# Performance work log

Hardware: AMD Instinct MI355X
Metric: run time of the kernel (lower is better)

Reference implementation:

```python
import jax, jax.numpy as jnp
import numpy as np
from jax import lax

NUM_NODES = 100000
FEAT = 256
RANK = 16
NNZ = 4000000
NUM_HE = 125000  # num_hyperedges == num_edges_total
K = 2000000      # int(0.5 * NNZ)


def setup_inputs() -> dict:
    key = jax.random.key(0)
    ks = jax.random.split(key, 6)
    x = jax.random.normal(ks[0], (NUM_NODES, FEAT), dtype=jnp.float32)
    W = jax.random.normal(ks[1], (RANK, FEAT), dtype=jnp.float32)
    edge_factors = jax.random.normal(ks[2], (NUM_HE, RANK), dtype=jnp.float32)
    V_idx = jax.random.randint(ks[3], (NNZ,), 0, NUM_NODES, dtype=jnp.int32)
    E_idx = jax.random.randint(ks[4], (NNZ,), 0, NUM_HE, dtype=jnp.int32)
    edge_ids = jax.random.randint(ks[5], (NUM_HE,), 0, NUM_HE, dtype=jnp.int32)
    return {"x": x, "W": W, "edge_factors": edge_factors,
            "V_idx": V_idx, "E_idx": E_idx, "edge_ids": edge_ids, "k": K}


def _segment_mean(vals, seg_ids, num_segments):
    s = jax.ops.segment_sum(vals, seg_ids, num_segments=num_segments)
    c = jax.ops.segment_sum(jnp.ones_like(vals), seg_ids, num_segments=num_segments)
    return s / jnp.maximum(c, 1.0)


def reference(x, W, edge_factors, V_idx, E_idx, edge_ids, k):
    # node_proj(x): [N, rank]; gather per-incidence node and edge factors, dot product
    proj = x @ W.T                                  # [N, rank]
    ef = edge_factors[edge_ids[E_idx]]              # [nnz, rank]
    logits = jnp.sum(proj[V_idx] * ef, axis=-1)     # [nnz]
    scores = jax.nn.sigmoid(logits)

    # is_test=True path: deterministic top-k keep set
    _, keep_ids = lax.top_k(scores, k)
    hard = jnp.zeros_like(scores).at[keep_ids].set(1.0)
    # straight-through: forward == hard, gradient flows through scores where hard==1
    soft = hard + (scores - lax.stop_gradient(scores)) * hard

    edge_probs = _segment_mean(lax.stop_gradient(scores), E_idx, NUM_HE)
    edge_soft = _segment_mean(soft, E_idx, NUM_HE)
    edge_hard = (_segment_mean(hard, E_idx, NUM_HE) > 0).astype(jnp.float32)
    return scores, soft, hard, edge_probs, edge_soft, edge_hard
```

## Files before the change

### kernel.cpp

```cpp
#include <hip/hip_runtime.h>
#include <math.h>

#define FEAT 256
#define RANKK 16
#define PRJ_NODES 16
#define CAND_CAP 131072
#define TIE_CAP 2048
#define NBK_MAX 512

typedef unsigned long long u64;

static __device__ __forceinline__ u64 pack_pair(unsigned e_low, unsigned bits, unsigned idx) {
    return ((u64)e_low << 56) | ((u64)bits << 26) | (u64)idx;
}

__global__ __launch_bounds__(256) void proj_kernel(const float* __restrict__ x,
        const float* __restrict__ Wm, float* __restrict__ proj, int n_nodes) {
    __shared__ float Ws[RANKK][FEAT + 4];
    __shared__ float Xs[PRJ_NODES][FEAT + 4];
    const float4* x4 = (const float4*)x;
    const float4* w4 = (const float4*)Wm;
    for (int t = threadIdx.x; t < RANKK * (FEAT / 4); t += 256) {
        int r = t >> 6, j4 = t & 63;
        *(float4*)&Ws[r][j4 * 4] = w4[t];
    }
    int nodeBase = blockIdx.x * PRJ_NODES;
    for (int t = threadIdx.x; t < PRJ_NODES * (FEAT / 4); t += 256) {
        int n = t >> 6, j4 = t & 63;
        int node = nodeBase + n;
        float4 v = make_float4(0.f, 0.f, 0.f, 0.f);
        if (node < n_nodes) v = x4[(size_t)node * (FEAT / 4) + j4];
        *(float4*)&Xs[n][j4 * 4] = v;
    }
    __syncthreads();
    int n = threadIdx.x >> 4, r = threadIdx.x & 15;
    int node = nodeBase + n;
    if (node >= n_nodes) return;
    double acc = 0.0;
    #pragma unroll 8
    for (int j4 = 0; j4 < FEAT / 4; ++j4) {
        float4 xv = *(const float4*)&Xs[n][j4 * 4];
        float4 wv = *(const float4*)&Ws[r][j4 * 4];
        acc += (double)xv.x * (double)wv.x + (double)xv.y * (double)wv.y
             + (double)xv.z * (double)wv.z + (double)xv.w * (double)wv.w;
    }
    proj[(size_t)node * RANKK + r] = (float)acc;
}

__global__ void gather_ef(const float4* __restrict__ ef, const int* __restrict__ edge_ids,
                          float4* __restrict__ ef2, int nhe) {
    int t = blockIdx.x * blockDim.x + threadIdx.x;
    if (t >= nhe * 4) return;
    int e = t >> 2, c = t & 3;
    ef2[(size_t)e * 4 + c] = ef[(size_t)edge_ids[e] * 4 + c];
}

__global__ void ehist_kernel(const int* __restrict__ E_idx, unsigned* __restrict__ bucketCnt,
                             int nnz, int nb) {
    __shared__ unsigned h[NBK_MAX];
    for (int t = threadIdx.x; t < NBK_MAX; t += blockDim.x) h[t] = 0;
    __syncthreads();
    for (int i = blockIdx.x * blockDim.x + threadIdx.x; i < nnz; i += gridDim.x * blockDim.x)
        atomicAdd(&h[((unsigned)E_idx[i]) >> 8], 1u);
    __syncthreads();
    for (int t = threadIdx.x; t < nb; t += blockDim.x)
        if (h[t]) atomicAdd(&bucketCnt[t], h[t]);
}

__global__ void bucket_scan(const unsigned* __restrict__ bucketCnt,
                            unsigned* __restrict__ bucketBase, unsigned* __restrict__ cursor,
                            int nb, int nnz) {
    __shared__ unsigned s[NBK_MAX];
    int t = threadIdx.x;
    unsigned c = (t < nb) ? bucketCnt[t] : 0u;
    s[t] = c;
    __syncthreads();
    for (int off = 1; off < NBK_MAX; off <<= 1) {
        unsigned v = (t >= off) ? s[t - off] : 0u;
        __syncthreads();
        s[t] += v;
        __syncthreads();
    }
    unsigned excl = s[t] - c;
    if (t < nb) { bucketBase[t] = excl; cursor[t] = excl; }
    if (t == 0) bucketBase[nb] = (unsigned)nnz;
}

__global__ __launch_bounds__(256) void score_kernel(
        const float4* __restrict__ proj4, const float4* __restrict__ ef4,
        const int2* __restrict__ V2, const int2* __restrict__ E2,
        float2* __restrict__ scores2, unsigned* __restrict__ hist1g,
        int npair, int nnz) {
    __shared__ unsigned h[4096];
    for (int t = threadIdx.x; t < 4096; t += 256) h[t] = 0;
    __syncthreads();
    unsigned r1016 = 0, r1015 = 0, r0 = 0;
    int stride = gridDim.x * 256;
    for (int i = blockIdx.x * 256 + threadIdx.x; i < npair; i += stride) {
        int2 v = V2[i];
        int2 e = E2[i];
        float4 a0 = proj4[(size_t)v.x * 4 + 0];
        float4 a1 = proj4[(size_t)v.x * 4 + 1];
        float4 a2 = proj4[(size_t)v.x * 4 + 2];
        float4 a3 = proj4[(size_t)v.x * 4 + 3];
        float4 b0 = proj4[(size_t)v.y * 4 + 0];
        float4 b1 = proj4[(size_t)v.y * 4 + 1];
        float4 b2 = proj4[(size_t)v.y * 4 + 2];
        float4 b3 = proj4[(size_t)v.y * 4 + 3];
        float4 f0 = ef4[(size_t)e.x * 4 + 0];
        float4 f1 = ef4[(size_t)e.x * 4 + 1];
        float4 f2 = ef4[(size_t)e.x * 4 + 2];
        float4 f3 = ef4[(size_t)e.x * 4 + 3];
        float4 g0 = ef4[(size_t)e.y * 4 + 0];
        float4 g1 = ef4[(size_t)e.y * 4 + 1];
        float4 g2 = ef4[(size_t)e.y * 4 + 2];
        float4 g3 = ef4[(size_t)e.y * 4 + 3];
        double acc0 = (double)a0.x * f0.x + (double)a0.y * f0.y + (double)a0.z * f0.z + (double)a0.w * f0.w
                    + (double)a1.x * f1.x + (double)a1.y * f1.y + (double)a1.z * f1.z + (double)a1.w * f1.w
                    + (double)a2.x * f2.x + (double)a2.y * f2.y + (double)a2.z * f2.z + (double)a2.w * f2.w
                    + (double)a3.x * f3.x + (double)a3.y * f3.y + (double)a3.z * f3.z + (double)a3.w * f3.w;
        double acc1 = (double)b0.x * g0.x + (double)b0.y * g0.y + (double)b0.z * g0.z + (double)b0.w * g0.w
                    + (double)b1.x * g1.x + (double)b1.y * g1.y + (double)b1.z * g1.z + (double)b1.w * g1.w
                    + (double)b2.x * g2.x + (double)b2.y * g2.y + (double)b2.z * g2.z + (double)b2.w * g2.w
                    + (double)b3.x * g3.x + (double)b3.y * g3.y + (double)b3.z * g3.z + (double)b3.w * g3.w;
        float s0 = (float)(1.0 / (1.0 + exp(-acc0)));
        float s1 = (float)(1.0 / (1.0 + exp(-acc1)));
        scores2[i] = make_float2(s0, s1);
        unsigned bb0 = __float_as_uint(s0) >> 20;
        unsigned bb1 = __float_as_uint(s1) >> 20;
        if (bb0 == 1016) ++r1016; else if (bb0 == 1015) ++r1015;
        else if (bb0 == 0) ++r0; else atomicAdd(&h[bb0], 1u);
        if (bb1 == 1016) ++r1016; else if (bb1 == 1015) ++r1015;
        else if (bb1 == 0) ++r0; else atomicAdd(&h[bb1], 1u);
    }
    if ((nnz & 1) && blockIdx.x == 0 && threadIdx.x == 0) {
        int i = nnz - 1;
        const int* Vi = (const int*)V2;
        const int* Ei = (const int*)E2;
        const float* pr = (const float*)proj4;
        const float* fr = (const float*)ef4;
        int v = Vi[i], e = Ei[i];
        double acc = 0.0;
        for (int r = 0; r < RANKK; ++r)
            acc += (double)pr[(size_t)v * RANKK + r] * (double)fr[(size_t)e * RANKK + r];
        float s = (float)(1.0 / (1.0 + exp(-acc)));
        ((float*)scores2)[i] = s;
        atomicAdd(&hist1g[__float_as_uint(s) >> 20], 1u);
    }
    if (r1016) atomicAdd(&h[1016], r1016);
    if (r1015) atomicAdd(&h[1015], r1015);
    if (r0) atomicAdd(&h[0], r0);
    __syncthreads();
    for (int t = threadIdx.x; t < 4096; t += 256)
        if (h[t]) atomicAdd(&hist1g[t], h[t]);
}

#define PB_CHUNK 8192
__global__ __launch_bounds__(256) void pair_build(const int* __restrict__ E_idx,
        const float* __restrict__ scores, u64* __restrict__ pairs,
        unsigned* __restrict__ cursor, int nnz, int nb) {
    __shared__ unsigned bh[NBK_MAX];
    for (int t = threadIdx.x; t < NBK_MAX; t += 256) bh[t] = 0;
    __syncthreads();
    int base = blockIdx.x * PB_CHUNK;
    int nE = nnz - base;
    if (nE > PB_CHUNK) nE = PB_CHUNK;
    for (int o = threadIdx.x; o < nE; o += 256)
        atomicAdd(&bh[((unsigned)E_idx[base + o]) >> 8], 1u);
    __syncthreads();
    for (int b = threadIdx.x; b < nb; b += 256) {
        unsigned c = bh[b];
        bh[b] = c ? atomicAdd(&cursor[b], c) : 0u;
    }
    __syncthreads();
    for (int o = threadIdx.x; o < nE; o += 256) {
        int i = base + o;
        unsigned e = (unsigned)E_idx[i];
        unsigned bits = __float_as_uint(scores[i]);
        unsigned pos = atomicAdd(&bh[e >> 8], 1u);
        pairs[pos] = pack_pair(e & 255u, bits, (unsigned)i);
    }
}

__global__ void scan1_kernel(const unsigned* __restrict__ hist,
                             unsigned* __restrict__ sel, const int* __restrict__ kptr) {
    __shared__ unsigned sfx[256];
    int t = threadIdx.x;
    unsigned local[16];
    unsigned s = 0;
    #pragma unroll
    for (int j = 0; j < 16; ++j) { local[j] = hist[t * 16 + j]; s += local[j]; }
    sfx[t] = s;
    __syncthreads();
    for (int off = 1; off < 256; off <<= 1) {
        unsigned add = (t + off < 256) ? sfx[t + off] : 0;
        __syncthreads();
        sfx[t] += add;
        __syncthreads();
    }
    unsigned krem = (unsigned)(*kptr);
    unsigned above = (t + 1 < 256) ? sfx[t + 1] : 0;
    if (above < krem && sfx[t] >= krem) {
        unsigned cum = above;
        int b = t * 16;
        for (int j = 15; j >= 0; --j) {
            unsigned cc = local[j];
            if (cum + cc >= krem) { b = t * 16 + j; break; }
            cum += cc;
        }
        sel[0] = krem - cum;
        sel[1] = ((unsigned)b) << 20;
    }
}

__global__ void compact_kernel(const float4* __restrict__ scores4,
                               const unsigned* __restrict__ sel,
                               uint2* __restrict__ cand, unsigned* __restrict__ candCount,
                               int n4, int nnz) {
    unsigned pref = sel[1] >> 20;
    int tid = blockIdx.x * blockDim.x + threadIdx.x;
    int stride = gridDim.x * blockDim.x;
    int lane = threadIdx.x & 63;
    int niter = (n4 + stride - 1) / stride;
    for (int kk = 0; kk < niter; ++kk) {
        int i = tid + kk * stride;
        bool inb = (i < n4);
        float4 sv = make_float4(0.f, 0.f, 0.f, 0.f);
        if (inb) sv = scores4[i];
        unsigned bb[4] = {__float_as_uint(sv.x), __float_as_uint(sv.y),
                          __float_as_uint(sv.z), __float_as_uint(sv.w)};
        #pragma unroll
        for (int q = 0; q < 4; ++q) {
            bool pred = inb && ((bb[q] >> 20) == pref);
            unsigned long long mask = __ballot(pred);
            if (mask) {
                int leader = __ffsll(mask) - 1;
                unsigned base = 0;
                if (lane == leader) base = atomicAdd(candCount, (unsigned)__popcll(mask));
                base = __shfl(base, leader, 64);
                if (pred) {
                    unsigned rank = __popcll(mask & ((1ull << lane) - 1ull));
                    unsigned pos = base + rank;
                    if (pos < CAND_CAP) cand[pos] = make_uint2(bb[q], (unsigned)(i * 4 + q));
                }
            }
        }
    }
    for (int i = n4 * 4 + tid; i < nnz; i += stride) {
        unsigned b = __float_as_uint(((const float*)scores4)[i]);
        if ((b >> 20) == pref) {
            unsigned pos = atomicAdd(candCount, 1u);
            if (pos < CAND_CAP) cand[pos] = make_uint2(b, (unsigned)i);
        }
    }
}

__global__ __launch_bounds__(256) void select_small(const uint2* __restrict__ cand,
                            const unsigned* __restrict__ candCount,
                            unsigned* __restrict__ sel, unsigned* __restrict__ tieList) {
    __shared__ unsigned h2[4096];
    __shared__ unsigned sfx[256];
    __shared__ unsigned sB2, sKrem2, sT, sM;
    __shared__ unsigned h3[256];
    __shared__ unsigned ties[TIE_CAP];
    __shared__ unsigned tcnt;
    int t = threadIdx.x;
    unsigned nc = *candCount;
    int n = (nc < CAND_CAP) ? (int)nc : CAND_CAP;
    unsigned krem = sel[0];
    unsigned pref = sel[1];

    for (int j = t; j < 4096; j += 256) h2[j] = 0;
    if (t == 0) tcnt = 0;
    __syncthreads();
    for (int j = t; j < n; j += 256) atomicAdd(&h2[(cand[j].x >> 8) & 0xFFF], 1u);
    __syncthreads();

    unsigned local[16];
    unsigned s = 0;
    #pragma unroll
    for (int j = 0; j < 16; ++j) { local[j] = h2[t * 16 + j]; s += local[j]; }
    sfx[t] = s;
    __syncthreads();
    for (int off = 1; off < 256; off <<= 1) {
        unsigned add = (t + off < 256) ? sfx[t + off] : 0;
        __syncthreads();
        sfx[t] += add;
        __syncthreads();
    }
    {
        unsigned above = (t + 1 < 256) ? sfx[t + 1] : 0;
        if (above < krem && sfx[t] >= krem) {
            unsigned cum = above;
            int b = t * 16;
            for (int j = 15; j >= 0; --j) {
                unsigned cc = local[j];
                if (cum + cc >= krem) { b = t * 16 + j; break; }
                cum += cc;
            }
            sB2 = (unsigned)b;
            sKrem2 = krem - cum;
        }
    }
    __syncthreads();

    h3[t] = 0;
    __syncthreads();
    unsigned b2 = sB2;
    for (int j = t; j < n; j += 256) {
        unsigned x = cand[j].x;
        if (((x >> 8) & 0xFFF) == b2) atomicAdd(&h3[x & 0xFF], 1u);
    }
    __syncthreads();
    sfx[t] = h3[t];
    __syncthreads();
    for (int off = 1; off < 256; off <<= 1) {
        unsigned add = (t + off < 256) ? sfx[t + off] : 0;
        __syncthreads();
        sfx[t] += add;
        __syncthreads();
    }
    {
        unsigned krem2 = sKrem2;
        unsigned above = (t + 1 < 256) ? sfx[t + 1] : 0;
        if (above < krem2 && sfx[t] >= krem2) {
            sT = pref | (b2 << 8) | (unsigned)t;
            sM = krem2 - above;
        }
    }
    __syncthreads();

    unsigned T = sT;
    for (int j = t; j < n; j += 256) {
        if (cand[j].x == T) {
            unsigned p = atomicAdd(&tcnt, 1u);
            if (p < TIE_CAP) ties[p] = cand[j].y;
        }
    }
    __syncthreads();
    if (t == 0) {
        unsigned cnt = (tcnt < TIE_CAP) ? tcnt : TIE_CAP;
        for (unsigned a = 1; a < cnt; ++a) {
            unsigned key = ties[a];
            int bpos = (int)a - 1;
            while (bpos >= 0 && ties[bpos] > key) { ties[bpos + 1] = ties[bpos]; --bpos; }
            ties[bpos + 1] = key;
        }
        unsigned m = sM;
        if (m > cnt) m = cnt;
        sel[2] = T;
        sel[3] = m;
        for (unsigned j = 0; j < m; ++j) tieList[j] = ties[j];
    }
}

__global__ __launch_bounds__(256) void edge_final(const u64* __restrict__ pairs,
        const unsigned* __restrict__ bucketBase, const unsigned* __restrict__ sel,
        const unsigned* __restrict__ tieList,
        float* __restrict__ eprob, float* __restrict__ esoft, float* __restrict__ ehard,
        int nhe) {
    __shared__ float ss[256];
    __shared__ unsigned cc[256];
    __shared__ unsigned hh[256];
    __shared__ unsigned ties[TIE_CAP];
    unsigned T = sel[2];
    unsigned m = sel[3];
    if (m > TIE_CAP) m = TIE_CAP;
    int t = threadIdx.x;
    ss[t] = 0.f; cc[t] = 0u; hh[t] = 0u;
    for (int j = t; j < (int)m; j += 256) ties[j] = tieList[j];
    __syncthreads();
    int b = blockIdx.x;
    unsigned n0 = bucketBase[b], n1 = bucketBase[b + 1];
    for (unsigned j = n0 + t; j < n1; j += 256) {
        u64 p = pairs[j];
        unsigned el = (unsigned)(p >> 56);
        unsigned bits = (unsigned)(p >> 26) & 0x3FFFFFFFu;
        atomicAdd(&ss[el], __uint_as_float(bits));
        atomicAdd(&cc[el], 1u);
        bool keep = bits > T;
        if (bits == T) {
            unsigned idx = (unsigned)(p & 0x3FFFFFFu);
            int lo = 0, hi = (int)m - 1;
            keep = false;
            while (lo <= hi) {
                int mid = (lo + hi) >> 1;
                unsigned v = ties[mid];
                if (v == idx) { keep = true; break; }
                if (v < idx) lo = mid + 1; else hi = mid - 1;
            }
        }
        if (keep) atomicAdd(&hh[el], 1u);
    }
    __syncthreads();
    int e = b * 256 + t;
    if (e < nhe) {
        float c = fmaxf((float)cc[t], 1.0f);
        eprob[e] = ss[t] / c;
        esoft[e] = (float)hh[t] / c;
        ehard[e] = (hh[t] > 0) ? 1.0f : 0.0f;
    }
}

__global__ __launch_bounds__(256) void write_hard(const float4* __restrict__ scores4,
                           const unsigned* __restrict__ sel,
                           const unsigned* __restrict__ tieList,
                           float4* __restrict__ hard4, float4* __restrict__ soft4,
                           int n4, int nnz) {
    __shared__ unsigned ties[TIE_CAP];
    unsigned T = sel[2];
    unsigned m = sel[3];
    if (m > TIE_CAP) m = TIE_CAP;
    for (int j = threadIdx.x; j < (int)m; j += blockDim.x) ties[j] = tieList[j];
    __syncthreads();
    int tid = blockIdx.x * blockDim.x + threadIdx.x;
    int stride = gridDim.x * blockDim.x;
    for (int i = tid; i < n4; i += stride) {
        float4 sv = scores4[i];
        unsigned bb[4] = {__float_as_uint(sv.x), __float_as_uint(sv.y),
                          __float_as_uint(sv.z), __float_as_uint(sv.w)};
        float hv[4];
        #pragma unroll
        for (int q = 0; q < 4; ++q) {
            bool keep = (bb[q] > T);
            if (bb[q] == T) {
                unsigned idx = (unsigned)(i * 4 + q);
                int lo = 0, hi = (int)m - 1;
                keep = false;
                while (lo <= hi) {
                    int mid = (lo + hi) >> 1;
                    unsigned v = ties[mid];
                    if (v == idx) { keep = true; break; }
                    if (v < idx) lo = mid + 1; else hi = mid - 1;
                }
            }
            hv[q] = keep ? 1.0f : 0.0f;
        }
        float4 outv = make_float4(hv[0], hv[1], hv[2], hv[3]);
        hard4[i] = outv;
        soft4[i] = outv;
    }
    const float* sc = (const float*)scores4;
    float* hard = (float*)hard4;
    float* soft = (float*)soft4;
    for (int i = n4 * 4 + tid; i < nnz; i += stride) {
        unsigned b = __float_as_uint(sc[i]);
        bool keep = (b > T);
        if (b == T) {
            unsigned idx = (unsigned)i;
            int lo = 0, hi = (int)m - 1;
            keep = false;
            while (lo <= hi) {
                int mid = (lo + hi) >> 1;
                unsigned v = ties[mid];
                if (v == idx) { keep = true; break; }
                if (v < idx) lo = mid + 1; else hi = mid - 1;
            }
        }
        float hvv = keep ? 1.0f : 0.0f;
        hard[i] = hvv;
        soft[i] = hvv;
    }
}

extern "C" void kernel_launch(void* const* d_in, const int* in_sizes, int n_in,
                              void* d_out, int out_size, void* d_ws, size_t ws_size,
                              hipStream_t stream) {
    const float* x        = (const float*)d_in[0];
    const float* Wm       = (const float*)d_in[1];
    const float* ef       = (const float*)d_in[2];
    const int*   V_idx    = (const int*)d_in[3];
    const int*   E_idx    = (const int*)d_in[4];
    const int*   edge_ids = (const int*)d_in[5];
    const int*   kptr     = (const int*)d_in[6];

    const int nnz     = in_sizes[3];
    const int nhe     = in_sizes[5];
    const int n_nodes = in_sizes[0] / FEAT;
    const int nb      = (nhe + 255) >> 8;

    float* out    = (float*)d_out;
    float* scores = out;
    float* soft   = out + (size_t)nnz;
    float* hard   = out + 2 * (size_t)nnz;
    float* eprob  = out + 3 * (size_t)nnz;
    float* esoft  = eprob + nhe;
    float* ehard  = esoft + nhe;

    u64*   pairs = (u64*)soft;
    uint2* cand  = (uint2*)eprob;

    char* w = (char*)d_ws;
    unsigned* hist1      = (unsigned*)w;
    unsigned* bucketCnt  = hist1 + 4096;
    unsigned* candCount  = bucketCnt + NBK_MAX;
    unsigned* sel        = candCount + 1;
    unsigned* tieList    = sel + 8;
    unsigned* bucketBase = tieList + TIE_CAP;
    unsigned* cursor     = bucketBase + NBK_MAX + 1;
    char* auxEnd = (char*)(cursor + NBK_MAX);
    size_t auxAligned = (((size_t)(auxEnd - w)) + 255) & ~(size_t)255;

    size_t ef2Bytes  = (size_t)nhe * RANKK * sizeof(float);
    size_t projBytes = (size_t)n_nodes * RANKK * sizeof(float);

    float* ef2;
    float* proj;
    if (ws_size >= auxAligned + ef2Bytes + projBytes) {
        ef2  = (float*)(w + auxAligned);
        proj = (float*)(w + auxAligned + ef2Bytes);
    } else {
        ef2  = hard;
        proj = hard + (size_t)nhe * RANKK;
    }

    hipMemsetAsync(w, 0, (size_t)(4096 + NBK_MAX + 1) * sizeof(unsigned), stream);

    ehist_kernel<<<128, 256, 0, stream>>>(E_idx, bucketCnt, nnz, nb);
    bucket_scan<<<1, NBK_MAX, 0, stream>>>(bucketCnt, bucketBase, cursor, nb, nnz);
    gather_ef<<<(nhe * 4 + 255) / 256, 256, 0, stream>>>(
        (const float4*)ef, edge_ids, (float4*)ef2, nhe);
    proj_kernel<<<(n_nodes + PRJ_NODES - 1) / PRJ_NODES, 256, 0, stream>>>(x, Wm, proj, n_nodes);

    int npair = nnz >> 1;
    score_kernel<<<2048, 256, 0, stream>>>(
        (const float4*)proj, (const float4*)ef2,
        (const int2*)V_idx, (const int2*)E_idx,
        (float2*)scores, hist1, npair, nnz);

    pair_build<<<(nnz + PB_CHUNK - 1) / PB_CHUNK, 256, 0, stream>>>(
        E_idx, scores, pairs, cursor, nnz, nb);

    int n4 = nnz / 4;
    scan1_kernel<<<1, 256, 0, stream>>>(hist1, sel, kptr);
    compact_kernel<<<1024, 256, 0, stream>>>(
        (const float4*)scores, sel, cand, candCount, n4, nnz);
    select_small<<<1, 256, 0, stream>>>(cand, candCount, sel, tieList);

    edge_final<<<nb, 256, 0, stream>>>(pairs, bucketBase, sel, tieList,
                                       eprob, esoft, ehard, nhe);
    write_hard<<<1024, 256, 0, stream>>>(
        (const float4*)scores, sel, tieList, (float4*)hard, (float4*)soft, n4, nnz);
}
```

Baseline: 539.8 us.

## Fuse small kernels with last-block ticket scans and merge gather/projection launches

Merges the edge histogram with its bucket scan using a last-block ticket, and merges the ef gather and node projection into one launch. The score histogram moves out of score_kernel into pair_build, and the top-k threshold scan now runs in the last block of that kernel. This cuts the number of launches and the serial single-block kernels. In exchange, score_kernel loses its paired int2 loads, pair_build rereads the scores for the histogram, and correctness now depends on threadfence/atomic ticket ordering.

```diff
diff --git a/kernel.cpp b/kernel.cpp
--- a/kernel.cpp
+++ b/kernel.cpp
@@ -7,6 +7,7 @@
 #define CAND_CAP 131072
 #define TIE_CAP 2048
 #define NBK_MAX 512
+#define PB_CHUNK 8192
 
 typedef unsigned long long u64;
 
@@ -14,17 +15,64 @@
     return ((u64)e_low << 56) | ((u64)bits << 26) | (u64)idx;
 }
 
-__global__ __launch_bounds__(256) void proj_kernel(const float* __restrict__ x,
-        const float* __restrict__ Wm, float* __restrict__ proj, int n_nodes) {
+__global__ __launch_bounds__(256) void ehist_scan(const int* __restrict__ E_idx,
+        unsigned* __restrict__ bucketCnt, unsigned* __restrict__ bucketBase,
+        unsigned* __restrict__ cursor, unsigned* __restrict__ ticket, int nnz) {
+    __shared__ unsigned h[NBK_MAX];
+    __shared__ unsigned ps[256];
+    __shared__ unsigned isLast;
+    int t = threadIdx.x;
+    for (int j = t; j < NBK_MAX; j += 256) h[j] = 0;
+    __syncthreads();
+    for (int i = blockIdx.x * 256 + t; i < nnz; i += gridDim.x * 256)
+        atomicAdd(&h[((unsigned)E_idx[i]) >> 8], 1u);
+    __syncthreads();
+    for (int j = t; j < NBK_MAX; j += 256)
+        if (h[j]) atomicAdd(&bucketCnt[j], h[j]);
+    __threadfence();
+    if (t == 0) isLast = (atomicAdd(ticket, 1u) == gridDim.x - 1) ? 1u : 0u;
+    __syncthreads();
+    if (!isLast) return;
+    unsigned a0 = atomicAdd(&bucketCnt[2 * t], 0u);
+    unsigned a1 = atomicAdd(&bucketCnt[2 * t + 1], 0u);
+    unsigned pairsum = a0 + a1;
+    ps[t] = pairsum;
+    __syncthreads();
+    for (int off = 1; off < 256; off <<= 1) {
+        unsigned v = (t >= off) ? ps[t - off] : 0u;
+        __syncthreads();
+        ps[t] += v;
+        __syncthreads();
+    }
+    unsigned excl = ps[t] - pairsum;
+    bucketBase[2 * t] = excl;           cursor[2 * t] = excl;
+    bucketBase[2 * t + 1] = excl + a0;  cursor[2 * t + 1] = excl + a0;
+    if (t == 255) bucketBase[NBK_MAX] = ps[255];
+}
+
+__global__ __launch_bounds__(256) void prep_combo(
+        const float4* __restrict__ ef, const int* __restrict__ edge_ids,
+        float4* __restrict__ ef2, int nhe,
+        const float* __restrict__ x, const float* __restrict__ Wm,
+        float* __restrict__ proj, int n_nodes, int G) {
     __shared__ float Ws[RANKK][FEAT + 4];
     __shared__ float Xs[PRJ_NODES][FEAT + 4];
+    if ((int)blockIdx.x < G) {
+        int t = blockIdx.x * 256 + threadIdx.x;
+        if (t < nhe * 4) {
+            int e = t >> 2, c = t & 3;
+            ef2[(size_t)e * 4 + c] = ef[(size_t)edge_ids[e] * 4 + c];
+        }
+        return;
+    }
+    int pb = blockIdx.x - G;
     const float4* x4 = (const float4*)x;
     const float4* w4 = (const float4*)Wm;
     for (int t = threadIdx.x; t < RANKK * (FEAT / 4); t += 256) {
         int r = t >> 6, j4 = t & 63;
         *(float4*)&Ws[r][j4 * 4] = w4[t];
     }
-    int nodeBase = blockIdx.x * PRJ_NODES;
+    int nodeBase = pb * PRJ_NODES;
     for (int t = threadIdx.x; t < PRJ_NODES * (FEAT / 4); t += 256) {
         int n = t >> 6, j4 = t & 63;
         int node = nodeBase + n;
@@ -47,149 +95,81 @@
     proj[(size_t)node * RANKK + r] = (float)acc;
 }
 
-__global__ void gather_ef(const float4* __restrict__ ef, const int* __restrict__ edge_ids,
-                          float4* __restrict__ ef2, int nhe) {
-    int t = blockIdx.x * blockDim.x + threadIdx.x;
-    if (t >= nhe * 4) return;
-    int e = t >> 2, c = t & 3;
-    ef2[(size_t)e * 4 + c] = ef[(size_t)edge_ids[e] * 4 + c];
-}
-
-__global__ void ehist_kernel(const int* __restrict__ E_idx, unsigned* __restrict__ bucketCnt,
-                             int nnz, int nb) {
-    __shared__ unsigned h[NBK_MAX];
-    for (int t = threadIdx.x; t < NBK_MAX; t += blockDim.x) h[t] = 0;
-    __syncthreads();
-    for (int i = blockIdx.x * blockDim.x + threadIdx.x; i < nnz; i += gridDim.x * blockDim.x)
-        atomicAdd(&h[((unsigned)E_idx[i]) >> 8], 1u);
-    __syncthreads();
-    for (int t = threadIdx.x; t < nb; t += blockDim.x)
-        if (h[t]) atomicAdd(&bucketCnt[t], h[t]);
-}
-
-__global__ void bucket_scan(const unsigned* __restrict__ bucketCnt,
-                            unsigned* __restrict__ bucketBase, unsigned* __restrict__ cursor,
-                            int nb, int nnz) {
-    __shared__ unsigned s[NBK_MAX];
-    int t = threadIdx.x;
-    unsigned c = (t < nb) ? bucketCnt[t] : 0u;
-    s[t] = c;
-    __syncthreads();
-    for (int off = 1; off < NBK_MAX; off <<= 1) {
-        unsigned v = (t >= off) ? s[t - off] : 0u;
-        __syncthreads();
-        s[t] += v;
-        __syncthreads();
-    }
-    unsigned excl = s[t] - c;
-    if (t < nb) { bucketBase[t] = excl; cursor[t] = excl; }
-    if (t == 0) bucketBase[nb] = (unsigned)nnz;
-}
-
 __global__ __launch_bounds__(256) void score_kernel(
         const float4* __restrict__ proj4, const float4* __restrict__ ef4,
-        const int2* __restrict__ V2, const int2* __restrict__ E2,
-        float2* __restrict__ scores2, unsigned* __restrict__ hist1g,
-        int npair, int nnz) {
+        const int* __restrict__ V_idx, const int* __restrict__ E_idx,
+        float* __restrict__ scores, int nnz) {
+    int stride = gridDim.x * blockDim.x;
+    #pragma unroll 2
+    for (int i = blockIdx.x * blockDim.x + threadIdx.x; i < nnz; i += stride) {
+        int v = V_idx[i], e = E_idx[i];
+        float4 p0 = proj4[(size_t)v * 4 + 0];
+        float4 p1 = proj4[(size_t)v * 4 + 1];
+        float4 p2 = proj4[(size_t)v * 4 + 2];
+        float4 p3 = proj4[(size_t)v * 4 + 3];
+        float4 f0 = ef4[(size_t)e * 4 + 0];
+        float4 f1 = ef4[(size_t)e * 4 + 1];
+        float4 f2 = ef4[(size_t)e * 4 + 2];
+        float4 f3 = ef4[(size_t)e * 4 + 3];
+        double acc = (double)p0.x * f0.x + (double)p0.y * f0.y + (double)p0.z * f0.z + (double)p0.w * f0.w
+                   + (double)p1.x * f1.x + (double)p1.y * f1.y + (double)p1.z * f1.z + (double)p1.w * f1.w
+                   + (double)p2.x * f2.x + (double)p2.y * f2.y + (double)p2.z * f2.z + (double)p2.w * f2.w
+                   + (double)p3.x * f3.x + (double)p3.y * f3.y + (double)p3.z * f3.z + (double)p3.w * f3.w;
+        scores[i] = (float)(1.0 / (1.0 + exp(-acc)));
+    }
+}
+
+__global__ __launch_bounds__(256) void pair_hist_scan(const int* __restrict__ E_idx,
+        const float* __restrict__ scores, u64* __restrict__ pairs,
+        unsigned* __restrict__ cursor, unsigned* __restrict__ hist1g,
+        unsigned* __restrict__ ticket, unsigned* __restrict__ sel,
+        const int* __restrict__ kptr, int nnz, int nb) {
+    __shared__ unsigned bh[NBK_MAX];
     __shared__ unsigned h[4096];
-    for (int t = threadIdx.x; t < 4096; t += 256) h[t] = 0;
-    __syncthreads();
+    __shared__ unsigned sfx[256];
+    __shared__ unsigned isLast;
+    int t = threadIdx.x;
+    for (int j = t; j < NBK_MAX; j += 256) bh[j] = 0;
+    for (int j = t; j < 4096; j += 256) h[j] = 0;
+    __syncthreads();
+    int base = blockIdx.x * PB_CHUNK;
+    int nE = nnz - base;
+    if (nE > PB_CHUNK) nE = PB_CHUNK;
     unsigned r1016 = 0, r1015 = 0, r0 = 0;
-    int stride = gridDim.x * 256;
-    for (int i = blockIdx.x * 256 + threadIdx.x; i < npair; i += stride) {
-        int2 v = V2[i];
-        int2 e = E2[i];
-        float4 a0 = proj4[(size_t)v.x * 4 + 0];
-        float4 a1 = proj4[(size_t)v.x * 4 + 1];
-        float4 a2 = proj4[(size_t)v.x * 4 + 2];
-        float4 a3 = proj4[(size_t)v.x * 4 + 3];
-        float4 b0 = proj4[(size_t)v.y * 4 + 0];
-        float4 b1 = proj4[(size_t)v.y * 4 + 1];
-        float4 b2 = proj4[(size_t)v.y * 4 + 2];
-        float4 b3 = proj4[(size_t)v.y * 4 + 3];
-        float4 f0 = ef4[(size_t)e.x * 4 + 0];
-        float4 f1 = ef4[(size_t)e.x * 4 + 1];
-        float4 f2 = ef4[(size_t)e.x * 4 + 2];
-        float4 f3 = ef4[(size_t)e.x * 4 + 3];
-        float4 g0 = ef4[(size_t)e.y * 4 + 0];
-        float4 g1 = ef4[(size_t)e.y * 4 + 1];
-        float4 g2 = ef4[(size_t)e.y * 4 + 2];
-        float4 g3 = ef4[(size_t)e.y * 4 + 3];
-        double acc0 = (double)a0.x * f0.x + (double)a0.y * f0.y + (double)a0.z * f0.z + (double)a0.w * f0.w
-                    + (double)a1.x * f1.x + (double)a1.y * f1.y + (double)a1.z * f1.z + (double)a1.w * f1.w
-                    + (double)a2.x * f2.x + (double)a2.y * f2.y + (double)a2.z * f2.z + (double)a2.w * f2.w
-                    + (double)a3.x * f3.x + (double)a3.y * f3.y + (double)a3.z * f3.z + (double)a3.w * f3.w;
-        double acc1 = (double)b0.x * g0.x + (double)b0.y * g0.y + (double)b0.z * g0.z + (double)b0.w * g0.w
-                    + (double)b1.x * g1.x + (double)b1.y * g1.y + (double)b1.z * g1.z + (double)b1.w * g1.w
-                    + (double)b2.x * g2.x + (double)b2.y * g2.y + (double)b2.z * g2.z + (double)b2.w * g2.w
-                    + (double)b3.x * g3.x + (double)b3.y * g3.y + (double)b3.z * g3.z + (double)b3.w * g3.w;
-        float s0 = (float)(1.0 / (1.0 + exp(-acc0)));
-        float s1 = (float)(1.0 / (1.0 + exp(-acc1)));
-        scores2[i] = make_float2(s0, s1);
-        unsigned bb0 = __float_as_uint(s0) >> 20;
-        unsigned bb1 = __float_as_uint(s1) >> 20;
-        if (bb0 == 1016) ++r1016; else if (bb0 == 1015) ++r1015;
-        else if (bb0 == 0) ++r0; else atomicAdd(&h[bb0], 1u);
-        if (bb1 == 1016) ++r1016; else if (bb1 == 1015) ++r1015;
-        else if (bb1 == 0) ++r0; else atomicAdd(&h[bb1], 1u);
-    }
-    if ((nnz & 1) && blockIdx.x == 0 && threadIdx.x == 0) {
-        int i = nnz - 1;
-        const int* Vi = (const int*)V2;
-        const int* Ei = (const int*)E2;
-        const float* pr = (const float*)proj4;
-        const float* fr = (const float*)ef4;
-        int v = Vi[i], e = Ei[i];
-        double acc = 0.0;
-        for (int r = 0; r < RANKK; ++r)
-            acc += (double)pr[(size_t)v * RANKK + r] * (double)fr[(size_t)e * RANKK + r];
-        float s = (float)(1.0 / (1.0 + exp(-acc)));
-        ((float*)scores2)[i] = s;
-        atomicAdd(&hist1g[__float_as_uint(s) >> 20], 1u);
+    for (int o = t; o < nE; o += 256) {
+        atomicAdd(&bh[((unsigned)E_idx[base + o]) >> 8], 1u);
+        unsigned b = __float_as_uint(scores[base + o]) >> 20;
+        if (b == 1016) ++r1016;
+        else if (b == 1015) ++r1015;
+        else if (b == 0) ++r0;
+        else atomicAdd(&h[b], 1u);
     }
     if (r1016) atomicAdd(&h[1016], r1016);
     if (r1015) atomicAdd(&h[1015], r1015);
     if (r0) atomicAdd(&h[0], r0);
     __syncthreads();
-    for (int t = threadIdx.x; t < 4096; t += 256)
-        if (h[t]) atomicAdd(&hist1g[t], h[t]);
-}
-
-#define PB_CHUNK 8192
-__global__ __launch_bounds__(256) void pair_build(const int* __restrict__ E_idx,
-        const float* __restrict__ scores, u64* __restrict__ pairs,
-        unsigned* __restrict__ cursor, int nnz, int nb) {
-    __shared__ unsigned bh[NBK_MAX];
-    for (int t = threadIdx.x; t < NBK_MAX; t += 256) bh[t] = 0;
-    __syncthreads();
-    int base = blockIdx.x * PB_CHUNK;
-    int nE = nnz - base;
-    if (nE > PB_CHUNK) nE = PB_CHUNK;
-    for (int o = threadIdx.x; o < nE; o += 256)
-        atomicAdd(&bh[((unsigned)E_idx[base + o]) >> 8], 1u);
-    __syncthreads();
-    for (int b = threadIdx.x; b < nb; b += 256) {
+    for (int b = t; b < nb; b += 256) {
         unsigned c = bh[b];
         bh[b] = c ? atomicAdd(&cursor[b], c) : 0u;
     }
-    __syncthreads();
-    for (int o = threadIdx.x; o < nE; o += 256) {
+    for (int j = t; j < 4096; j += 256)
+        if (h[j]) atomicAdd(&hist1g[j], h[j]);
+    __syncthreads();
+    for (int o = t; o < nE; o += 256) {
         int i = base + o;
         unsigned e = (unsigned)E_idx[i];
         unsigned bits = __float_as_uint(scores[i]);
         unsigned pos = atomicAdd(&bh[e >> 8], 1u);
         pairs[pos] = pack_pair(e & 255u, bits, (unsigned)i);
     }
-}
-
-__global__ void scan1_kernel(const unsigned* __restrict__ hist,
-                             unsigned* __restrict__ sel, const int* __restrict__ kptr) {
-    __shared__ unsigned sfx[256];
-    int t = threadIdx.x;
+    __threadfence();
+    if (t == 0) isLast = (atomicAdd(ticket, 1u) == gridDim.x - 1) ? 1u : 0u;
+    __syncthreads();
+    if (!isLast) return;
     unsigned local[16];
     unsigned s = 0;
     #pragma unroll
-    for (int j = 0; j < 16; ++j) { local[j] = hist[t * 16 + j]; s += local[j]; }
+    for (int j = 0; j < 16; ++j) { local[j] = atomicAdd(&hist1g[t * 16 + j], 0u); s += local[j]; }
     sfx[t] = s;
     __syncthreads();
     for (int off = 1; off < 256; off <<= 1) {
@@ -494,12 +474,15 @@
     unsigned* hist1      = (unsigned*)w;
     unsigned* bucketCnt  = hist1 + 4096;
     unsigned* candCount  = bucketCnt + NBK_MAX;
-    unsigned* sel        = candCount + 1;
+    unsigned* ticket1    = candCount + 1;
+    unsigned* ticket2    = ticket1 + 1;
+    unsigned* sel        = ticket2 + 1;
     unsigned* tieList    = sel + 8;
     unsigned* bucketBase = tieList + TIE_CAP;
     unsigned* cursor     = bucketBase + NBK_MAX + 1;
     char* auxEnd = (char*)(cursor + NBK_MAX);
     size_t auxAligned = (((size_t)(auxEnd - w)) + 255) & ~(size_t)255;
+    size_t zeroBytes = (size_t)(4096 + NBK_MAX + 3) * sizeof(unsigned);
 
     size_t ef2Bytes  = (size_t)nhe * RANKK * sizeof(float);
     size_t projBytes = (size_t)n_nodes * RANKK * sizeof(float);
@@ -514,25 +497,22 @@
         proj = hard + (size_t)nhe * RANKK;
     }
 
-    hipMemsetAsync(w, 0, (size_t)(4096 + NBK_MAX + 1) * sizeof(unsigned), stream);
-
-    ehist_kernel<<<128, 256, 0, stream>>>(E_idx, bucketCnt, nnz, nb);
-    bucket_scan<<<1, NBK_MAX, 0, stream>>>(bucketCnt, bucketBase, cursor, nb, nnz);
-    gather_ef<<<(nhe * 4 + 255) / 256, 256, 0, stream>>>(
-        (const float4*)ef, edge_ids, (float4*)ef2, nhe);
-    proj_kernel<<<(n_nodes + PRJ_NODES - 1) / PRJ_NODES, 256, 0, stream>>>(x, Wm, proj, n_nodes);
-
-    int npair = nnz >> 1;
+    hipMemsetAsync(w, 0, zeroBytes, stream);
+
+    ehist_scan<<<128, 256, 0, stream>>>(E_idx, bucketCnt, bucketBase, cursor, ticket1, nnz);
+
+    int G = (nhe * 4 + 255) / 256;
+    int P = (n_nodes + PRJ_NODES - 1) / PRJ_NODES;
+    prep_combo<<<G + P, 256, 0, stream>>>((const float4*)ef, edge_ids, (float4*)ef2, nhe,
+                                          x, Wm, proj, n_nodes, G);
+
     score_kernel<<<2048, 256, 0, stream>>>(
-        (const float4*)proj, (const float4*)ef2,
-        (const int2*)V_idx, (const int2*)E_idx,
-        (float2*)scores, hist1, npair, nnz);
-
-    pair_build<<<(nnz + PB_CHUNK - 1) / PB_CHUNK, 256, 0, stream>>>(
-        E_idx, scores, pairs, cursor, nnz, nb);
+        (const float4*)proj, (const float4*)ef2, V_idx, E_idx, scores, nnz);
+
+    pair_hist_scan<<<(nnz + PB_CHUNK - 1) / PB_CHUNK, 256, 0, stream>>>(
+        E_idx, scores, pairs, cursor, hist1, ticket2, sel, kptr, nnz, nb);
 
     int n4 = nnz / 4;
-    scan1_kernel<<<1, 256, 0, stream>>>(hist1, sel, kptr);
     compact_kernel<<<1024, 256, 0, stream>>>(
         (const float4*)scores, sel, cand, candCount, n4, nnz);
     select_small<<<1, 256, 0, stream>>>(cand, candCount, sel, tieList);
```

New measurement: 570.5 us. +5.7%, slower.
